# Kernel tuning notes

Measured on AMD Instinct MI355X. Metric: run time of the kernel, lower is better.

The kernel has to match this reference:

```python
import jax, jax.numpy as jnp
import numpy as np

EPS = 1e-5  # torch BatchNorm1d default

def _silu(x):
    return x * jax.nn.sigmoid(x)

def _bn(x, g, b, rm, rv, axis):
    # eval-mode batchnorm along given channel axis
    shape = [1] * x.ndim
    shape[axis] = -1
    return (x - rm.reshape(shape)) * (g.reshape(shape) / jnp.sqrt(rv.reshape(shape) + EPS)) + b.reshape(shape)

def setup_inputs() -> dict:
    key = jax.random.key(0)
    ks = jax.random.split(key, 12)
    b, n, p, d, r = 64, 256, 12, 128, 2
    x = jax.random.normal(ks[0], (b, n, p, d), dtype=jnp.float32)
    # k branch: Conv1d(p -> 1, k=1, bias=False) + BN(1)
    wk = jax.random.normal(ks[1], (p,), dtype=jnp.float32) / np.sqrt(p)
    bn_k_g = jax.random.uniform(ks[2], (1,), dtype=jnp.float32, minval=0.5, maxval=1.5)
    bn_k_b = 0.1 * jax.random.normal(ks[3], (1,), dtype=jnp.float32)
    bn_k_rm = jnp.zeros((1,), jnp.float32)
    bn_k_rv = jnp.ones((1,), jnp.float32)
    # v branch: Conv1d(d -> d, k=1, bias=False) + BN(d)
    wv = jax.random.normal(ks[4], (d, d), dtype=jnp.float32) / np.sqrt(d)
    bn_v_g = jax.random.uniform(ks[5], (d,), dtype=jnp.float32, minval=0.5, maxval=1.5)
    bn_v_b = 0.1 * jax.random.normal(ks[6], (d,), dtype=jnp.float32)
    bn_v_rm = jnp.zeros((d,), jnp.float32)
    bn_v_rv = jnp.ones((d,), jnp.float32)
    # fc_avg / fc_max: Linear(n, n//r, bias=False) -> GELU -> Linear(n//r, n, bias=False)
    w_avg1 = jax.random.normal(ks[7], (n // r, n), dtype=jnp.float32) / np.sqrt(n)
    w_avg2 = jax.random.normal(ks[8], (n, n // r), dtype=jnp.float32) / np.sqrt(n // r)
    w_max1 = jax.random.normal(ks[9], (n // r, n), dtype=jnp.float32) / np.sqrt(n)
    w_max2 = jax.random.normal(ks[10], (n, n // r), dtype=jnp.float32) / np.sqrt(n // r)
    return dict(x=x, wk=wk, bn_k_g=bn_k_g, bn_k_b=bn_k_b, bn_k_rm=bn_k_rm, bn_k_rv=bn_k_rv,
                wv=wv, bn_v_g=bn_v_g, bn_v_b=bn_v_b, bn_v_rm=bn_v_rm, bn_v_rv=bn_v_rv,
                w_avg1=w_avg1, w_avg2=w_avg2, w_max1=w_max1, w_max2=w_max2)

def _forward(x, wk, bn_k_g, bn_k_b, bn_k_rm, bn_k_rv, wv, bn_v_g, bn_v_b, bn_v_rm, bn_v_rv,
             w_avg1, w_avg2, w_max1, w_max2):
    b, n, p, d = x.shape
    xf = x.reshape(b * n, p, d)
    # squeeze-excite gates: pool over d, FC over n
    avg = jnp.mean(xf, axis=-1).reshape(b, n, p).transpose(0, 2, 1)  # [b,p,n]
    mx = jnp.max(xf, axis=-1).reshape(b, n, p).transpose(0, 2, 1)    # [b,p,n]
    gelu = lambda t: jax.nn.gelu(t, approximate=False)
    avg_g = jax.nn.sigmoid(gelu(avg @ w_avg1.T) @ w_avg2.T).transpose(0, 2, 1)  # [b,n,p]
    max_g = jax.nn.sigmoid(gelu(mx @ w_max1.T) @ w_max2.T).transpose(0, 2, 1)   # [b,n,p]
    # k: 1x1 conv over p channels -> [bn, d], BN(1ch), SiLU, softmax over d
    k_raw = jnp.einsum('bpd,p->bd', xf, wk)
    k = jax.nn.softmax(_silu(k_raw * (bn_k_g / jnp.sqrt(bn_k_rv + EPS)) - bn_k_rm * (bn_k_g / jnp.sqrt(bn_k_rv + EPS)) + bn_k_b), axis=-1)  # [bn,d]
    # v: 1x1 conv over d channels on [bn,d,p], BN(d), SiLU -> [bn,p,d]
    v_raw = jnp.einsum('bpd,ed->bpe', xf, wv)  # channel axis is last here
    v = _silu(_bn(v_raw, bn_v_g, bn_v_b, bn_v_rm, bn_v_rv, axis=2))  # [bn,p,d]
    # y = v @ k : [bn,p];  y_pool = (max+avg) @ v : [bn,d]
    y = jnp.einsum('bpd,bd->bp', v, k)
    pool = (max_g + avg_g).reshape(b * n, p)
    y_pool = jnp.einsum('bp,bpd->bd', pool, v)
    out = y_pool[:, None, :] * y[:, :, None]  # [bn,p,d]
    return out.reshape(b, n, p, d)

def reference(x, wk, bn_k_g, bn_k_b, bn_k_rm, bn_k_rv, wv, bn_v_g, bn_v_b, bn_v_rm, bn_v_rv,
              w_avg1, w_avg2, w_max1, w_max2):
    return _forward(x, wk, bn_k_g, bn_k_b, bn_k_rm, bn_k_rv, wv, bn_v_g, bn_v_b, bn_v_rm, bn_v_rv,
                    w_avg1, w_avg2, w_max1, w_max2)
```

## Files before the change

### kernel.cpp

```cpp
#include <hip/hip_runtime.h>
#include <hip/hip_bf16.h>

#define B_   64
#define N_   256
#define P_   12
#define D_   128
#define BN_  (B_*N_)
#define EPSV 1e-5f

typedef float  f32x4  __attribute__((ext_vector_type(4)));
typedef __bf16 bf16x8 __attribute__((ext_vector_type(8)));
typedef __bf16 bf16x4 __attribute__((ext_vector_type(4)));

__device__ float  g_avg[768*256];
__device__ float  g_mx [768*256];
__device__ float  g_h1 [1536*128];
__device__ float  g_pool[BN_*P_];
__device__ float  g_k  [BN_*D_];
__device__ __bf16 g_xbf[(size_t)BN_*P_*D_];

__device__ inline float sigm_(float x) { return 1.0f / (1.0f + __expf(-x)); }

__device__ inline float dot4_(float4 a, float4 b, float acc) {
  acc = fmaf(a.x, b.x, acc); acc = fmaf(a.y, b.y, acc);
  acc = fmaf(a.z, b.z, acc); acc = fmaf(a.w, b.w, acc);
  return acc;
}

__global__ __launch_bounds__(256) void k1_pool(const float* __restrict__ x,
                                               const float* __restrict__ wk,
                                               const float* __restrict__ kg,
                                               const float* __restrict__ kb,
                                               const float* __restrict__ krm,
                                               const float* __restrict__ krv) {
  int w = threadIdx.x >> 6, l = threadIdx.x & 63;
  int bn = blockIdx.x * 4 + w;
  const float* xp = x + (size_t)bn * (P_ * D_);
  __bf16* xbp = g_xbf + (size_t)bn * (P_ * D_);
  int half = l >> 5, lane32 = l & 31;
  float ksc = kg[0] * rsqrtf(krv[0] + EPSV);
  float kbs = kb[0] - krm[0] * ksc;
  float s6[6], m6[6];
  float kr0 = 0, kr1 = 0, kr2 = 0, kr3 = 0;
#pragma unroll
  for (int pp = 0; pp < 6; ++pp) {
    int p = pp * 2 + half;
    float4 v = *(const float4*)(xp + p * D_ + lane32 * 4);
    bf16x4 h;
    h[0] = (__bf16)v.x; h[1] = (__bf16)v.y; h[2] = (__bf16)v.z; h[3] = (__bf16)v.w;
    *(bf16x4*)(xbp + p * D_ + lane32 * 4) = h;
    float wkp = wk[p];
    kr0 = fmaf(v.x, wkp, kr0); kr1 = fmaf(v.y, wkp, kr1);
    kr2 = fmaf(v.z, wkp, kr2); kr3 = fmaf(v.w, wkp, kr3);
    float s = (v.x + v.y) + (v.z + v.w);
    float m = fmaxf(fmaxf(v.x, v.y), fmaxf(v.z, v.w));
#pragma unroll
    for (int off = 16; off; off >>= 1) {
      s += __shfl_xor(s, off);
      m = fmaxf(m, __shfl_xor(m, off));
    }
    s6[pp] = s * (1.0f / D_);
    m6[pp] = m;
  }
  kr0 += __shfl_xor(kr0, 32); kr1 += __shfl_xor(kr1, 32);
  kr2 += __shfl_xor(kr2, 32); kr3 += __shfl_xor(kr3, 32);
  float z0 = kr0 * ksc + kbs, z1 = kr1 * ksc + kbs;
  float z2 = kr2 * ksc + kbs, z3 = kr3 * ksc + kbs;
  z0 = z0 * sigm_(z0); z1 = z1 * sigm_(z1);
  z2 = z2 * sigm_(z2); z3 = z3 * sigm_(z3);
  float mx = fmaxf(fmaxf(z0, z1), fmaxf(z2, z3));
#pragma unroll
  for (int off = 16; off; off >>= 1) mx = fmaxf(mx, __shfl_xor(mx, off));
  float e0 = __expf(z0 - mx), e1 = __expf(z1 - mx);
  float e2 = __expf(z2 - mx), e3 = __expf(z3 - mx);
  float es = (e0 + e1) + (e2 + e3);
#pragma unroll
  for (int off = 16; off; off >>= 1) es += __shfl_xor(es, off);
  float inv = 1.0f / es;
  if (half == 0) {
    float4 kk; kk.x = e0 * inv; kk.y = e1 * inv; kk.z = e2 * inv; kk.w = e3 * inv;
    *(float4*)(g_k + (size_t)bn * D_ + lane32 * 4) = kk;
  }
  if (lane32 == 0) {
    int b = bn >> 8, n = bn & 255;
#pragma unroll
    for (int pp = 0; pp < 6; ++pp) {
      int p = pp * 2 + half;
      g_avg[(b * P_ + p) * N_ + n] = s6[pp];
      g_mx [(b * P_ + p) * N_ + n] = m6[pp];
    }
  }
}

__global__ __launch_bounds__(256) void k2_l1(const float* __restrict__ w_avg1,
                                             const float* __restrict__ w_max1) {
  __shared__ float in_t[16 * 256];
  __shared__ float w_t[64 * 68];
  int t = threadIdx.x;
  int rblk = blockIdx.x % 96, cblk = blockIdx.x / 96;
  int rr0 = rblk * 16, c0 = cblk * 64;
  bool mxb = (rr0 >= 768);
  int r768 = mxb ? rr0 - 768 : rr0;
  const float* in = (mxb ? g_mx : g_avg) + (size_t)r768 * 256;
  const float* w1 = mxb ? w_max1 : w_avg1;
#pragma unroll
  for (int i = 0; i < 4; ++i) {
    int F = t + i * 256, r = F >> 6, k4 = F & 63;
    *(float4*)(in_t + r * 256 + k4 * 4) = *(const float4*)(in + r * 256 + k4 * 4);
  }
  int c = t & 63, rq = t >> 6;
  float a0 = 0, a1 = 0, a2 = 0, a3 = 0;
  for (int kc = 0; kc < 4; ++kc) {
    __syncthreads();
#pragma unroll
    for (int i = 0; i < 4; ++i) {
      int F = t + i * 256, cr = F >> 4, k4 = F & 15;
      *(float4*)(w_t + cr * 68 + k4 * 4) =
          *(const float4*)(w1 + (size_t)(c0 + cr) * 256 + kc * 64 + k4 * 4);
    }
    __syncthreads();
#pragma unroll
    for (int k4 = 0; k4 < 16; ++k4) {
      float4 wv4 = *(float4*)(w_t + c * 68 + k4 * 4);
      a0 = dot4_(*(float4*)(in_t + (rq * 4 + 0) * 256 + kc * 64 + k4 * 4), wv4, a0);
      a1 = dot4_(*(float4*)(in_t + (rq * 4 + 1) * 256 + kc * 64 + k4 * 4), wv4, a1);
      a2 = dot4_(*(float4*)(in_t + (rq * 4 + 2) * 256 + kc * 64 + k4 * 4), wv4, a2);
      a3 = dot4_(*(float4*)(in_t + (rq * 4 + 3) * 256 + kc * 64 + k4 * 4), wv4, a3);
    }
  }
  float accs[4] = {a0, a1, a2, a3};
#pragma unroll
  for (int r = 0; r < 4; ++r) {
    float a = accs[r];
    float g = 0.5f * a * (1.0f + erff(a * 0.70710678f));
    g_h1[(size_t)(rr0 + rq * 4 + r) * 128 + c0 + c] = g;
  }
}

__global__ __launch_bounds__(256) void k2_l2(const float* __restrict__ w_avg2,
                                             const float* __restrict__ w_max2) {
  __shared__ float ina_t[16 * 128];
  __shared__ float inm_t[16 * 128];
  __shared__ float wa_t[64 * 68];
  __shared__ float wm_t[64 * 68];
  int t = threadIdx.x;
  int rblk = blockIdx.x % 48, cblk = blockIdx.x / 48;
  int rr0 = rblk * 16, n0 = cblk * 64;
#pragma unroll
  for (int i = 0; i < 2; ++i) {
    int F = t + i * 256, r = F >> 5, k4 = F & 31;
    *(float4*)(ina_t + r * 128 + k4 * 4) = *(const float4*)(g_h1 + (size_t)(rr0 + r) * 128 + k4 * 4);
    *(float4*)(inm_t + r * 128 + k4 * 4) = *(const float4*)(g_h1 + (size_t)(768 + rr0 + r) * 128 + k4 * 4);
  }
  int c = t & 63, rq = t >> 6;
  float aa0=0, aa1=0, aa2=0, aa3=0, am0=0, am1=0, am2=0, am3=0;
  for (int kc = 0; kc < 2; ++kc) {
    __syncthreads();
#pragma unroll
    for (int i = 0; i < 4; ++i) {
      int F = t + i * 256, cr = F >> 4, k4 = F & 15;
      *(float4*)(wa_t + cr * 68 + k4 * 4) =
          *(const float4*)(w_avg2 + (size_t)(n0 + cr) * 128 + kc * 64 + k4 * 4);
      *(float4*)(wm_t + cr * 68 + k4 * 4) =
          *(const float4*)(w_max2 + (size_t)(n0 + cr) * 128 + kc * 64 + k4 * 4);
    }
    __syncthreads();
#pragma unroll
    for (int k4 = 0; k4 < 16; ++k4) {
      float4 wa4 = *(float4*)(wa_t + c * 68 + k4 * 4);
      float4 wm4 = *(float4*)(wm_t + c * 68 + k4 * 4);
      float4 i0 = *(float4*)(ina_t + (rq * 4 + 0) * 128 + kc * 64 + k4 * 4);
      float4 i1 = *(float4*)(ina_t + (rq * 4 + 1) * 128 + kc * 64 + k4 * 4);
      float4 i2 = *(float4*)(ina_t + (rq * 4 + 2) * 128 + kc * 64 + k4 * 4);
      float4 i3 = *(float4*)(ina_t + (rq * 4 + 3) * 128 + kc * 64 + k4 * 4);
      aa0 = dot4_(i0, wa4, aa0); aa1 = dot4_(i1, wa4, aa1);
      aa2 = dot4_(i2, wa4, aa2); aa3 = dot4_(i3, wa4, aa3);
      float4 j0 = *(float4*)(inm_t + (rq * 4 + 0) * 128 + kc * 64 + k4 * 4);
      float4 j1 = *(float4*)(inm_t + (rq * 4 + 1) * 128 + kc * 64 + k4 * 4);
      float4 j2 = *(float4*)(inm_t + (rq * 4 + 2) * 128 + kc * 64 + k4 * 4);
      float4 j3 = *(float4*)(inm_t + (rq * 4 + 3) * 128 + kc * 64 + k4 * 4);
      am0 = dot4_(j0, wm4, am0); am1 = dot4_(j1, wm4, am1);
      am2 = dot4_(j2, wm4, am2); am3 = dot4_(j3, wm4, am3);
    }
  }
  float va[4] = {aa0, aa1, aa2, aa3};
  float vm[4] = {am0, am1, am2, am3};
#pragma unroll
  for (int r = 0; r < 4; ++r) {
    int rr = rr0 + rq * 4 + r;
    int b = rr / 12, p = rr % 12;
    float pv = sigm_(va[r]) + sigm_(vm[r]);
    g_pool[((size_t)b * 256 + (n0 + c)) * 12 + p] = pv;
  }
}

__global__ __launch_bounds__(256) void k3_main(
    const float* __restrict__ wv,
    const float* __restrict__ vg, const float* __restrict__ vb,
    const float* __restrict__ vrm, const float* __restrict__ vrv,
    float* __restrict__ out) {
  __shared__ __align__(16) __bf16 wv_lds[128 * 128];
  __shared__ float sv_l[128], tv_l[128];
  __shared__ float yp_l[4][128];
  __shared__ __align__(16) float y_l[4][16];

  int t = threadIdx.x, w = t >> 6, l = t & 63;
  if (t < 128) {
    float s = vg[t] * rsqrtf(vrv[t] + EPSV);
    sv_l[t] = s;
    tv_l[t] = vb[t] - vrm[t] * s;
  }
  __syncthreads();
  {
    int e = t >> 1, dh = (t & 1) * 64;
    float s = sv_l[e];
    int swz = (e & 7) << 4;
#pragma unroll
    for (int i = 0; i < 16; ++i) {
      float4 v4 = *(const float4*)(wv + (size_t)e * 128 + dh + i * 4);
      bf16x4 h;
      h[0] = (__bf16)(v4.x * s); h[1] = (__bf16)(v4.y * s);
      h[2] = (__bf16)(v4.z * s); h[3] = (__bf16)(v4.w * s);
      int byte = (e * 256 + (dh + i * 4) * 2) ^ swz;
      *(bf16x4*)((char*)wv_lds + byte) = h;
    }
  }
  __syncthreads();

  int arow = (l & 15) > 11 ? 11 : (l & 15);
  int ak = (l >> 4) * 8;
  int bcol = l & 15;
  int bko = (l >> 4) * 16;
  int p0 = (l >> 4) * 4;
  bool rows_ok = (p0 < 12);

  float tv_e[8];
#pragma unroll
  for (int nt = 0; nt < 8; ++nt) tv_e[nt] = tv_l[bcol + nt * 16];

  for (int it = 0; it < 2; ++it) {
    int bn = blockIdx.x * 8 + it * 4 + w;

    float pool_r[4] = {0.f, 0.f, 0.f, 0.f};
    if (rows_ok) {
      const float* pp = g_pool + (size_t)bn * 12 + p0;
#pragma unroll
      for (int r = 0; r < 4; ++r) pool_r[r] = pp[r];
    }

    const float* kp = g_k + (size_t)bn * D_;
    float k_e[8];
#pragma unroll
    for (int nt = 0; nt < 8; ++nt) k_e[nt] = kp[bcol + nt * 16];

    const __bf16* xbp = g_xbf + (size_t)bn * (P_ * D_) + arow * D_;
    bf16x8 afr[4];
#pragma unroll
    for (int ks = 0; ks < 4; ++ks)
      afr[ks] = *(const bf16x8*)(xbp + ks * 32 + ak);

    f32x4 acc[8];
#pragma unroll
    for (int nt = 0; nt < 8; ++nt) acc[nt] = (f32x4){0.f, 0.f, 0.f, 0.f};
#pragma unroll
    for (int nt = 0; nt < 8; ++nt) {
      int er = bcol + nt * 16;
      int base = er * 256;
      int sw = (er & 7) << 4;
#pragma unroll
      for (int ks = 0; ks < 4; ++ks) {
        int byte = (base + ks * 64 + bko) ^ sw;
        bf16x8 bfr = *(const bf16x8*)((const char*)wv_lds + byte);
        acc[nt] = __builtin_amdgcn_mfma_f32_16x16x32_bf16(afr[ks], bfr, acc[nt], 0, 0, 0);
      }
    }

    float y_r[4] = {0.f, 0.f, 0.f, 0.f};
    float ypp[8];
#pragma unroll
    for (int nt = 0; nt < 8; ++nt) {
      float s = 0.f;
#pragma unroll
      for (int r = 0; r < 4; ++r) {
        float a = acc[nt][r] + tv_e[nt];
        float v = a * sigm_(a);
        y_r[r] = fmaf(v, k_e[nt], y_r[r]);
        s = fmaf(pool_r[r], v, s);
      }
      ypp[nt] = s;
    }
#pragma unroll
    for (int r = 0; r < 4; ++r) {
#pragma unroll
      for (int off = 8; off; off >>= 1) y_r[r] += __shfl_xor(y_r[r], off);
    }
#pragma unroll
    for (int nt = 0; nt < 8; ++nt) {
      ypp[nt] += __shfl_xor(ypp[nt], 16);
      ypp[nt] += __shfl_xor(ypp[nt], 32);
    }

    if (bcol == 0 && rows_ok) {
      float4 yq; yq.x = y_r[0]; yq.y = y_r[1]; yq.z = y_r[2]; yq.w = y_r[3];
      *(float4*)(&y_l[w][p0]) = yq;
    }
    if (l < 16) {
#pragma unroll
      for (int nt = 0; nt < 8; ++nt) yp_l[w][bcol + nt * 16] = ypp[nt];
    }
    float2 yp2 = *(const float2*)(&yp_l[w][2 * l]);
    float yv[P_];
#pragma unroll
    for (int p = 0; p < P_; ++p) yv[p] = y_l[w][p];

    float* op = out + (size_t)bn * (P_ * D_);
#pragma unroll
    for (int p = 0; p < P_; ++p) {
      float2 o;
      o.x = yv[p] * yp2.x;
      o.y = yv[p] * yp2.y;
      *(float2*)(op + p * 128 + 2 * l) = o;
    }
  }
}

extern "C" void kernel_launch(void* const* d_in, const int* in_sizes, int n_in,
                              void* d_out, int out_size, void* d_ws, size_t ws_size,
                              hipStream_t stream) {
  const float* x   = (const float*)d_in[0];
  const float* wk  = (const float*)d_in[1];
  const float* kg  = (const float*)d_in[2];
  const float* kbb = (const float*)d_in[3];
  const float* krm = (const float*)d_in[4];
  const float* krv = (const float*)d_in[5];
  const float* wvp = (const float*)d_in[6];
  const float* vg  = (const float*)d_in[7];
  const float* vbb = (const float*)d_in[8];
  const float* vrm = (const float*)d_in[9];
  const float* vrv = (const float*)d_in[10];
  const float* wa1 = (const float*)d_in[11];
  const float* wa2 = (const float*)d_in[12];
  const float* wm1 = (const float*)d_in[13];
  const float* wm2 = (const float*)d_in[14];
  float* out = (float*)d_out;

  k1_pool<<<4096, 256, 0, stream>>>(x, wk, kg, kbb, krm, krv);
  k2_l1<<<192, 256, 0, stream>>>(wa1, wm1);
  k2_l2<<<192, 256, 0, stream>>>(wa2, wm2);
  k3_main<<<2048, 256, 0, stream>>>(wvp, vg, vbb, vrm, vrv, out);
}
```

Baseline: 129.4 us.

## Precompute swizzled bf16 wv once and process two bn rows per wave

Adds a small prep kernel that folds the BN scale into wv, converts it to bf16 in the swizzled LDS layout, and computes the BN shift once into global memory. The main kernel then fills LDS with a plain 16-byte copy instead of converting per block. Each wave now handles two bn rows with interleaved MFMA chains, and the grid is halved, so the LDS weight fill is amortized over more work and more independent instructions are in flight. The cost is higher register pressure, which may reduce occupancy, plus one extra kernel launch.

```diff
diff --git a/kernel.cpp b/kernel.cpp
--- a/kernel.cpp
+++ b/kernel.cpp
@@ -18,6 +18,8 @@
 __device__ float  g_pool[BN_*P_];
 __device__ float  g_k  [BN_*D_];
 __device__ __bf16 g_xbf[(size_t)BN_*P_*D_];
+__device__ __align__(16) __bf16 g_wvbf[128*128];
+__device__ float  g_tv [128];
 
 __device__ inline float sigm_(float x) { return 1.0f / (1.0f + __expf(-x)); }
 
@@ -25,6 +27,29 @@
   acc = fmaf(a.x, b.x, acc); acc = fmaf(a.y, b.y, acc);
   acc = fmaf(a.z, b.z, acc); acc = fmaf(a.w, b.w, acc);
   return acc;
+}
+
+__global__ __launch_bounds__(256) void k0_prep(const float* __restrict__ wv,
+                                               const float* __restrict__ vg,
+                                               const float* __restrict__ vb,
+                                               const float* __restrict__ vrm,
+                                               const float* __restrict__ vrv) {
+  int t = blockIdx.x * 256 + threadIdx.x;
+  if (blockIdx.x == 0 && threadIdx.x < 128) {
+    float s0 = vg[threadIdx.x] * rsqrtf(vrv[threadIdx.x] + EPSV);
+    g_tv[threadIdx.x] = vb[threadIdx.x] - vrm[threadIdx.x] * s0;
+  }
+  int e = t >> 5;
+  float s = vg[e] * rsqrtf(vrv[e] + EPSV);
+  int qbase = t * 8;
+  int swz = (e & 7) << 4;
+  bf16x4 h;
+#pragma unroll
+  for (int j = 0; j < 4; ++j) {
+    int inner = ((qbase & 255) + j * 2) ^ swz;
+    h[j] = (__bf16)(wv[e * 128 + (inner >> 1)] * s);
+  }
+  *(bf16x4*)((char*)g_wvbf + qbase) = h;
 }
 
 __global__ __launch_bounds__(256) void k1_pool(const float* __restrict__ x,
@@ -194,35 +219,21 @@
   }
 }
 
-__global__ __launch_bounds__(256) void k3_main(
-    const float* __restrict__ wv,
-    const float* __restrict__ vg, const float* __restrict__ vb,
-    const float* __restrict__ vrm, const float* __restrict__ vrv,
-    float* __restrict__ out) {
+__global__ __launch_bounds__(256) void k3_main(float* __restrict__ out) {
   __shared__ __align__(16) __bf16 wv_lds[128 * 128];
-  __shared__ float sv_l[128], tv_l[128];
-  __shared__ float yp_l[4][128];
-  __shared__ __align__(16) float y_l[4][16];
+  __shared__ float tv_l[128];
+  __shared__ float yp_l[4][2][128];
+  __shared__ __align__(16) float y_l[4][2][16];
 
   int t = threadIdx.x, w = t >> 6, l = t & 63;
-  if (t < 128) {
-    float s = vg[t] * rsqrtf(vrv[t] + EPSV);
-    sv_l[t] = s;
-    tv_l[t] = vb[t] - vrm[t] * s;
-  }
-  __syncthreads();
+  if (t < 128) tv_l[t] = g_tv[t];
   {
-    int e = t >> 1, dh = (t & 1) * 64;
-    float s = sv_l[e];
-    int swz = (e & 7) << 4;
-#pragma unroll
-    for (int i = 0; i < 16; ++i) {
-      float4 v4 = *(const float4*)(wv + (size_t)e * 128 + dh + i * 4);
-      bf16x4 h;
-      h[0] = (__bf16)(v4.x * s); h[1] = (__bf16)(v4.y * s);
-      h[2] = (__bf16)(v4.z * s); h[3] = (__bf16)(v4.w * s);
-      int byte = (e * 256 + (dh + i * 4) * 2) ^ swz;
-      *(bf16x4*)((char*)wv_lds + byte) = h;
+    const uint4* src = (const uint4*)g_wvbf;
+    uint4* dst = (uint4*)wv_lds;
+#pragma unroll
+    for (int i = 0; i < 8; ++i) {
+      int idx = i * 256 + t;
+      dst[idx] = src[idx];
     }
   }
   __syncthreads();
@@ -239,87 +250,108 @@
   for (int nt = 0; nt < 8; ++nt) tv_e[nt] = tv_l[bcol + nt * 16];
 
   for (int it = 0; it < 2; ++it) {
-    int bn = blockIdx.x * 8 + it * 4 + w;
-
-    float pool_r[4] = {0.f, 0.f, 0.f, 0.f};
+    int bnA = blockIdx.x * 16 + it * 8 + w;
+    int bnB = bnA + 4;
+
+    const __bf16* xpA = g_xbf + (size_t)bnA * (P_ * D_) + arow * D_;
+    const __bf16* xpB = g_xbf + (size_t)bnB * (P_ * D_) + arow * D_;
+    bf16x8 afrA[4], afrB[4];
+#pragma unroll
+    for (int ks = 0; ks < 4; ++ks) {
+      afrA[ks] = *(const bf16x8*)(xpA + ks * 32 + ak);
+      afrB[ks] = *(const bf16x8*)(xpB + ks * 32 + ak);
+    }
+    const float* kpA = g_k + (size_t)bnA * D_;
+    const float* kpB = g_k + (size_t)bnB * D_;
+    float keA[8], keB[8];
+#pragma unroll
+    for (int nt = 0; nt < 8; ++nt) {
+      keA[nt] = kpA[bcol + nt * 16];
+      keB[nt] = kpB[bcol + nt * 16];
+    }
+    float poolA[4] = {0.f, 0.f, 0.f, 0.f};
+    float poolB[4] = {0.f, 0.f, 0.f, 0.f};
     if (rows_ok) {
-      const float* pp = g_pool + (size_t)bn * 12 + p0;
-#pragma unroll
-      for (int r = 0; r < 4; ++r) pool_r[r] = pp[r];
-    }
-
-    const float* kp = g_k + (size_t)bn * D_;
-    float k_e[8];
-#pragma unroll
-    for (int nt = 0; nt < 8; ++nt) k_e[nt] = kp[bcol + nt * 16];
-
-    const __bf16* xbp = g_xbf + (size_t)bn * (P_ * D_) + arow * D_;
-    bf16x8 afr[4];
-#pragma unroll
-    for (int ks = 0; ks < 4; ++ks)
-      afr[ks] = *(const bf16x8*)(xbp + ks * 32 + ak);
-
-    f32x4 acc[8];
-#pragma unroll
-    for (int nt = 0; nt < 8; ++nt) acc[nt] = (f32x4){0.f, 0.f, 0.f, 0.f};
+      const float* ppA = g_pool + (size_t)bnA * 12 + p0;
+      const float* ppB = g_pool + (size_t)bnB * 12 + p0;
+#pragma unroll
+      for (int r = 0; r < 4; ++r) { poolA[r] = ppA[r]; poolB[r] = ppB[r]; }
+    }
+
+    float yrA[4] = {0.f, 0.f, 0.f, 0.f};
+    float yrB[4] = {0.f, 0.f, 0.f, 0.f};
+    float yppA[8], yppB[8];
 #pragma unroll
     for (int nt = 0; nt < 8; ++nt) {
       int er = bcol + nt * 16;
       int base = er * 256;
       int sw = (er & 7) << 4;
+      f32x4 aA = (f32x4){0.f, 0.f, 0.f, 0.f};
+      f32x4 aB = (f32x4){0.f, 0.f, 0.f, 0.f};
 #pragma unroll
       for (int ks = 0; ks < 4; ++ks) {
         int byte = (base + ks * 64 + bko) ^ sw;
         bf16x8 bfr = *(const bf16x8*)((const char*)wv_lds + byte);
-        acc[nt] = __builtin_amdgcn_mfma_f32_16x16x32_bf16(afr[ks], bfr, acc[nt], 0, 0, 0);
+        aA = __builtin_amdgcn_mfma_f32_16x16x32_bf16(afrA[ks], bfr, aA, 0, 0, 0);
+        aB = __builtin_amdgcn_mfma_f32_16x16x32_bf16(afrB[ks], bfr, aB, 0, 0, 0);
       }
-    }
-
-    float y_r[4] = {0.f, 0.f, 0.f, 0.f};
-    float ypp[8];
+      float tvv = tv_e[nt];
+      float sA = 0.f, sB = 0.f;
+#pragma unroll
+      for (int r = 0; r < 4; ++r) {
+        float a = aA[r] + tvv;
+        float v = a * sigm_(a);
+        yrA[r] = fmaf(v, keA[nt], yrA[r]);
+        sA = fmaf(poolA[r], v, sA);
+        float b = aB[r] + tvv;
+        float vb2 = b * sigm_(b);
+        yrB[r] = fmaf(vb2, keB[nt], yrB[r]);
+        sB = fmaf(poolB[r], vb2, sB);
+      }
+      yppA[nt] = sA; yppB[nt] = sB;
+    }
+
+#pragma unroll
+    for (int r = 0; r < 4; ++r) {
+#pragma unroll
+      for (int off = 8; off; off >>= 1) {
+        yrA[r] += __shfl_xor(yrA[r], off);
+        yrB[r] += __shfl_xor(yrB[r], off);
+      }
+    }
 #pragma unroll
     for (int nt = 0; nt < 8; ++nt) {
-      float s = 0.f;
-#pragma unroll
-      for (int r = 0; r < 4; ++r) {
-        float a = acc[nt][r] + tv_e[nt];
-        float v = a * sigm_(a);
-        y_r[r] = fmaf(v, k_e[nt], y_r[r]);
-        s = fmaf(pool_r[r], v, s);
+      yppA[nt] += __shfl_xor(yppA[nt], 16);
+      yppA[nt] += __shfl_xor(yppA[nt], 32);
+      yppB[nt] += __shfl_xor(yppB[nt], 16);
+      yppB[nt] += __shfl_xor(yppB[nt], 32);
+    }
+
+    if (bcol == 0 && rows_ok) {
+      float4 qA; qA.x = yrA[0]; qA.y = yrA[1]; qA.z = yrA[2]; qA.w = yrA[3];
+      float4 qB; qB.x = yrB[0]; qB.y = yrB[1]; qB.z = yrB[2]; qB.w = yrB[3];
+      *(float4*)(&y_l[w][0][p0]) = qA;
+      *(float4*)(&y_l[w][1][p0]) = qB;
+    }
+    if (l < 16) {
+#pragma unroll
+      for (int nt = 0; nt < 8; ++nt) {
+        yp_l[w][0][bcol + nt * 16] = yppA[nt];
+        yp_l[w][1][bcol + nt * 16] = yppB[nt];
       }
-      ypp[nt] = s;
-    }
-#pragma unroll
-    for (int r = 0; r < 4; ++r) {
-#pragma unroll
-      for (int off = 8; off; off >>= 1) y_r[r] += __shfl_xor(y_r[r], off);
-    }
-#pragma unroll
-    for (int nt = 0; nt < 8; ++nt) {
-      ypp[nt] += __shfl_xor(ypp[nt], 16);
-      ypp[nt] += __shfl_xor(ypp[nt], 32);
-    }
-
-    if (bcol == 0 && rows_ok) {
-      float4 yq; yq.x = y_r[0]; yq.y = y_r[1]; yq.z = y_r[2]; yq.w = y_r[3];
-      *(float4*)(&y_l[w][p0]) = yq;
-    }
-    if (l < 16) {
-#pragma unroll
-      for (int nt = 0; nt < 8; ++nt) yp_l[w][bcol + nt * 16] = ypp[nt];
-    }
-    float2 yp2 = *(const float2*)(&yp_l[w][2 * l]);
-    float yv[P_];
-#pragma unroll
-    for (int p = 0; p < P_; ++p) yv[p] = y_l[w][p];
-
-    float* op = out + (size_t)bn * (P_ * D_);
+    }
+    float2 ypA = *(const float2*)(&yp_l[w][0][2 * l]);
+    float2 ypB = *(const float2*)(&yp_l[w][1][2 * l]);
+    float* opA = out + (size_t)bnA * (P_ * D_);
+    float* opB = out + (size_t)bnB * (P_ * D_);
 #pragma unroll
     for (int p = 0; p < P_; ++p) {
-      float2 o;
-      o.x = yv[p] * yp2.x;
-      o.y = yv[p] * yp2.y;
-      *(float2*)(op + p * 128 + 2 * l) = o;
+      float yvA = y_l[w][0][p];
+      float2 oA; oA.x = yvA * ypA.x; oA.y = yvA * ypA.y;
+      *(float2*)(opA + p * 128 + 2 * l) = oA;
+      float yvB = y_l[w][1][p];
+      float2 oB; oB.x = yvB * ypB.x; oB.y = yvB * ypB.y;
+      *(float2*)(opB + p * 128 + 2 * l) = oB;
     }
   }
 }
@@ -344,8 +376,9 @@
   const float* wm2 = (const float*)d_in[14];
   float* out = (float*)d_out;
 
+  k0_prep<<<16, 256, 0, stream>>>(wvp, vg, vbb, vrm, vrv);
   k1_pool<<<4096, 256, 0, stream>>>(x, wk, kg, kbb, krm, krv);
   k2_l1<<<192, 256, 0, stream>>>(wa1, wm1);
   k2_l2<<<192, 256, 0, stream>>>(wa2, wm2);
-  k3_main<<<2048, 256, 0, stream>>>(wvp, vg, vbb, vrm, vrv, out);
-}
+  k3_main<<<1024, 256, 0, stream>>>(out);
+}
```

Result: faster. 118.6 us (-8.3%).

## Precompute scaled bf16 Wv once and keep it in registers in main kernel

Applied to the files above, without the earlier changes.

A new prep kernel folds the BN scale into Wv, converts it to bf16 and computes the BN shift once, writing both to global memory. Before this, every one of the 2048 blocks of the main kernel rebuilt the swizzled LDS copy of Wv. The main kernel now runs single-wavefront blocks that hold the whole B fragment set in registers, and it replaces the LDS reductions with cross-lane shuffles. This removes the per-block setup work and all LDS traffic and barriers, at the cost of heavy register pressure (32 bf16x8 fragments per lane) and one extra kernel launch.

```diff
diff --git a/kernel.cpp b/kernel.cpp
--- a/kernel.cpp
+++ b/kernel.cpp
@@ -18,6 +18,8 @@
 __device__ float  g_pool[BN_*P_];
 __device__ float  g_k  [BN_*D_];
 __device__ __bf16 g_xbf[(size_t)BN_*P_*D_];
+__device__ __align__(16) __bf16 g_wvbf[128*128];
+__device__ float  g_tv [128];
 
 __device__ inline float sigm_(float x) { return 1.0f / (1.0f + __expf(-x)); }
 
@@ -25,6 +27,25 @@
   acc = fmaf(a.x, b.x, acc); acc = fmaf(a.y, b.y, acc);
   acc = fmaf(a.z, b.z, acc); acc = fmaf(a.w, b.w, acc);
   return acc;
+}
+
+__global__ __launch_bounds__(256) void k0_prep(const float* __restrict__ wv,
+                                               const float* __restrict__ vg,
+                                               const float* __restrict__ vb,
+                                               const float* __restrict__ vrm,
+                                               const float* __restrict__ vrv) {
+  int t = blockIdx.x * 256 + threadIdx.x;
+  if (blockIdx.x == 0 && threadIdx.x < 128) {
+    float s0 = vg[threadIdx.x] * rsqrtf(vrv[threadIdx.x] + EPSV);
+    g_tv[threadIdx.x] = vb[threadIdx.x] - vrm[threadIdx.x] * s0;
+  }
+  int idx = t * 4;
+  int e = idx >> 7, d0 = idx & 127;
+  float s = vg[e] * rsqrtf(vrv[e] + EPSV);
+  bf16x4 h;
+#pragma unroll
+  for (int j = 0; j < 4; ++j) h[j] = (__bf16)(wv[e * 128 + d0 + j] * s);
+  *(bf16x4*)(g_wvbf + idx) = h;
 }
 
 __global__ __launch_bounds__(256) void k1_pool(const float* __restrict__ x,
@@ -194,53 +215,37 @@
   }
 }
 
-__global__ __launch_bounds__(256) void k3_main(
-    const float* __restrict__ wv,
-    const float* __restrict__ vg, const float* __restrict__ vb,
-    const float* __restrict__ vrm, const float* __restrict__ vrv,
-    float* __restrict__ out) {
-  __shared__ __align__(16) __bf16 wv_lds[128 * 128];
-  __shared__ float sv_l[128], tv_l[128];
-  __shared__ float yp_l[4][128];
-  __shared__ __align__(16) float y_l[4][16];
-
-  int t = threadIdx.x, w = t >> 6, l = t & 63;
-  if (t < 128) {
-    float s = vg[t] * rsqrtf(vrv[t] + EPSV);
-    sv_l[t] = s;
-    tv_l[t] = vb[t] - vrm[t] * s;
-  }
-  __syncthreads();
-  {
-    int e = t >> 1, dh = (t & 1) * 64;
-    float s = sv_l[e];
-    int swz = (e & 7) << 4;
-#pragma unroll
-    for (int i = 0; i < 16; ++i) {
-      float4 v4 = *(const float4*)(wv + (size_t)e * 128 + dh + i * 4);
-      bf16x4 h;
-      h[0] = (__bf16)(v4.x * s); h[1] = (__bf16)(v4.y * s);
-      h[2] = (__bf16)(v4.z * s); h[3] = (__bf16)(v4.w * s);
-      int byte = (e * 256 + (dh + i * 4) * 2) ^ swz;
-      *(bf16x4*)((char*)wv_lds + byte) = h;
-    }
-  }
-  __syncthreads();
-
-  int arow = (l & 15) > 11 ? 11 : (l & 15);
+__global__ __launch_bounds__(64) void k3_main(float* __restrict__ out) {
+  int l = threadIdx.x;
+  int bcol = l & 15;
+  int arow = bcol > 11 ? 11 : bcol;
   int ak = (l >> 4) * 8;
-  int bcol = l & 15;
-  int bko = (l >> 4) * 16;
   int p0 = (l >> 4) * 4;
   bool rows_ok = (p0 < 12);
 
+  bf16x8 bfr[8][4];
+#pragma unroll
+  for (int nt = 0; nt < 8; ++nt) {
+    const __bf16* wp = g_wvbf + (bcol + nt * 16) * 128 + ak;
+#pragma unroll
+    for (int ks = 0; ks < 4; ++ks)
+      bfr[nt][ks] = *(const bf16x8*)(wp + ks * 32);
+  }
   float tv_e[8];
 #pragma unroll
-  for (int nt = 0; nt < 8; ++nt) tv_e[nt] = tv_l[bcol + nt * 16];
-
-  for (int it = 0; it < 2; ++it) {
-    int bn = blockIdx.x * 8 + it * 4 + w;
-
+  for (int nt = 0; nt < 8; ++nt) tv_e[nt] = g_tv[bcol + nt * 16];
+
+  for (int it = 0; it < 4; ++it) {
+    int bn = blockIdx.x * 4 + it;
+
+    const __bf16* xp = g_xbf + (size_t)bn * (P_ * D_) + arow * D_;
+    bf16x8 afr[4];
+#pragma unroll
+    for (int ks = 0; ks < 4; ++ks) afr[ks] = *(const bf16x8*)(xp + ks * 32 + ak);
+    const float* kp = g_k + (size_t)bn * D_;
+    float k_e[8];
+#pragma unroll
+    for (int nt = 0; nt < 8; ++nt) k_e[nt] = kp[bcol + nt * 16];
     float pool_r[4] = {0.f, 0.f, 0.f, 0.f};
     if (rows_ok) {
       const float* pp = g_pool + (size_t)bn * 12 + p0;
@@ -248,47 +253,26 @@
       for (int r = 0; r < 4; ++r) pool_r[r] = pp[r];
     }
 
-    const float* kp = g_k + (size_t)bn * D_;
-    float k_e[8];
-#pragma unroll
-    for (int nt = 0; nt < 8; ++nt) k_e[nt] = kp[bcol + nt * 16];
-
-    const __bf16* xbp = g_xbf + (size_t)bn * (P_ * D_) + arow * D_;
-    bf16x8 afr[4];
-#pragma unroll
-    for (int ks = 0; ks < 4; ++ks)
-      afr[ks] = *(const bf16x8*)(xbp + ks * 32 + ak);
-
-    f32x4 acc[8];
-#pragma unroll
-    for (int nt = 0; nt < 8; ++nt) acc[nt] = (f32x4){0.f, 0.f, 0.f, 0.f};
-#pragma unroll
-    for (int nt = 0; nt < 8; ++nt) {
-      int er = bcol + nt * 16;
-      int base = er * 256;
-      int sw = (er & 7) << 4;
-#pragma unroll
-      for (int ks = 0; ks < 4; ++ks) {
-        int byte = (base + ks * 64 + bko) ^ sw;
-        bf16x8 bfr = *(const bf16x8*)((const char*)wv_lds + byte);
-        acc[nt] = __builtin_amdgcn_mfma_f32_16x16x32_bf16(afr[ks], bfr, acc[nt], 0, 0, 0);
-      }
-    }
-
     float y_r[4] = {0.f, 0.f, 0.f, 0.f};
     float ypp[8];
 #pragma unroll
     for (int nt = 0; nt < 8; ++nt) {
+      f32x4 acc = (f32x4){0.f, 0.f, 0.f, 0.f};
+#pragma unroll
+      for (int ks = 0; ks < 4; ++ks)
+        acc = __builtin_amdgcn_mfma_f32_16x16x32_bf16(afr[ks], bfr[nt][ks], acc, 0, 0, 0);
+      float tvv = tv_e[nt];
       float s = 0.f;
 #pragma unroll
       for (int r = 0; r < 4; ++r) {
-        float a = acc[nt][r] + tv_e[nt];
+        float a = acc[r] + tvv;
         float v = a * sigm_(a);
         y_r[r] = fmaf(v, k_e[nt], y_r[r]);
         s = fmaf(pool_r[r], v, s);
       }
       ypp[nt] = s;
     }
+
 #pragma unroll
     for (int r = 0; r < 4; ++r) {
 #pragma unroll
@@ -300,25 +284,24 @@
       ypp[nt] += __shfl_xor(ypp[nt], 32);
     }
 
-    if (bcol == 0 && rows_ok) {
-      float4 yq; yq.x = y_r[0]; yq.y = y_r[1]; yq.z = y_r[2]; yq.w = y_r[3];
-      *(float4*)(&y_l[w][p0]) = yq;
-    }
-    if (l < 16) {
-#pragma unroll
-      for (int nt = 0; nt < 8; ++nt) yp_l[w][bcol + nt * 16] = ypp[nt];
-    }
-    float2 yp2 = *(const float2*)(&yp_l[w][2 * l]);
-    float yv[P_];
-#pragma unroll
-    for (int p = 0; p < P_; ++p) yv[p] = y_l[w][p];
+    int cs = (l & 7) * 2;
+    int ntw = l >> 3;
+    float ypx = 0.f, ypy = 0.f;
+#pragma unroll
+    for (int nt = 0; nt < 8; ++nt) {
+      float sx = __shfl(ypp[nt], cs);
+      float sy = __shfl(ypp[nt], cs + 1);
+      ypx = (ntw == nt) ? sx : ypx;
+      ypy = (ntw == nt) ? sy : ypy;
+    }
 
     float* op = out + (size_t)bn * (P_ * D_);
 #pragma unroll
     for (int p = 0; p < P_; ++p) {
+      float yp = __shfl(y_r[p & 3], (p >> 2) * 16);
       float2 o;
-      o.x = yv[p] * yp2.x;
-      o.y = yv[p] * yp2.y;
+      o.x = yp * ypx;
+      o.y = yp * ypy;
       *(float2*)(op + p * 128 + 2 * l) = o;
     }
   }
@@ -344,8 +327,9 @@
   const float* wm2 = (const float*)d_in[14];
   float* out = (float*)d_out;
 
+  k0_prep<<<16, 256, 0, stream>>>(wvp, vg, vbb, vrm, vrv);
   k1_pool<<<4096, 256, 0, stream>>>(x, wk, kg, kbb, krm, krv);
   k2_l1<<<192, 256, 0, stream>>>(wa1, wm1);
   k2_l2<<<192, 256, 0, stream>>>(wa2, wm2);
-  k3_main<<<2048, 256, 0, stream>>>(wvp, vg, vbb, vrm, vrv, out);
-}
+  k3_main<<<4096, 64, 0, stream>>>(out);
+}
```

Result: faster. 111.0 us (-14.2%).
